# Optimization experiments

Measured on AMD Instinct MI355X. Metric: run time of the kernel, lower is better.

## Reference

```python
import jax, jax.numpy as jnp
import numpy as np

B, S, D, H = 2, 2048, 1024, 16
HD = D // H  # head_dim = 64


def setup_inputs() -> dict:
    key = jax.random.key(0)
    ks = jax.random.split(key, 10)
    std = 1.0 / np.sqrt(D)
    inputs = jax.random.normal(ks[0], (B, S, D), dtype=jnp.float32)
    # stacked per-head projection weights: [H, HD, D] (row-major like nn.Linear)
    Wq = jax.random.uniform(ks[1], (H, HD, D), jnp.float32, -std, std)
    bq = jax.random.uniform(ks[2], (H, HD), jnp.float32, -std, std)
    Wk = jax.random.uniform(ks[3], (H, HD, D), jnp.float32, -std, std)
    bk = jax.random.uniform(ks[4], (H, HD), jnp.float32, -std, std)
    Wv = jax.random.uniform(ks[5], (H, HD, D), jnp.float32, -std, std)
    bv = jax.random.uniform(ks[6], (H, HD), jnp.float32, -std, std)
    Wo = jax.random.uniform(ks[7], (D, D), jnp.float32, -std, std)
    bo = jax.random.uniform(ks[8], (D,), jnp.float32, -std, std)
    return {"inputs": inputs, "Wq": Wq, "bq": bq, "Wk": Wk, "bk": bk,
            "Wv": Wv, "bv": bv, "Wo": Wo, "bo": bo}


def reference(inputs, Wq, bq, Wk, bk, Wv, bv, Wo, bo):
    # per-head projections, batched over heads: [B,H,S,HD]
    q = jnp.einsum('bsd,hed->bhse', inputs, Wq) + bq[None, :, None, :]
    k = jnp.einsum('bsd,hed->bhse', inputs, Wk) + bk[None, :, None, :]
    v = jnp.einsum('bsd,hed->bhse', inputs, Wv) + bv[None, :, None, :]
    scale = 1.0 / np.sqrt(HD).astype(np.float32)
    # explicit [B,H,S,S] score matrix, as in the original naive attention
    scores = jnp.einsum('bhqe,bhke->bhqk', q, k) * scale
    causal = jnp.tril(jnp.ones((S, S), dtype=bool))
    scores = jnp.where(causal[None, None], scores, jnp.float32(-jnp.inf))
    attn = jax.nn.softmax(scores, axis=-1)  # dropout p=0 -> identity
    wv = jnp.einsum('bhqk,bhke->bhqe', attn, v)
    # concat heads along feature dim: [B,S,H*HD] = [B,S,D]
    z = wv.transpose(0, 2, 1, 3).reshape(B, S, D)
    out = jnp.einsum('bsd,ed->bse', z, Wo) + bo
    return out
```

## Files before the change

### kernel.cpp

```cpp
#include <hip/hip_runtime.h>
#include <math.h>

#define Bx 2
#define Sx 2048
#define Dx 1024
#define Hx 16
#define HDx 64
#define Mx (Bx*Sx)

typedef __bf16 bf16x8 __attribute__((ext_vector_type(8)));
typedef __bf16 bf16x4 __attribute__((ext_vector_type(4)));
typedef float  f32x4  __attribute__((ext_vector_type(4)));

#define SCL 0.18033688011112042f

__device__ __forceinline__ void gload_lds16(const __bf16* g, __bf16* l) {
  __builtin_amdgcn_global_load_lds(
      (const __attribute__((address_space(1))) unsigned int*)g,
      (__attribute__((address_space(3))) unsigned int*)l, 16, 0, 0);
}

__device__ __forceinline__ void cvt8(const float* s, __bf16* d) {
  float4 a = *(const float4*)s;
  float4 b = *(const float4*)(s + 4);
  bf16x8 o;
  o[0] = (__bf16)a.x; o[1] = (__bf16)a.y; o[2] = (__bf16)a.z; o[3] = (__bf16)a.w;
  o[4] = (__bf16)b.x; o[5] = (__bf16)b.y; o[6] = (__bf16)b.z; o[7] = (__bf16)b.w;
  *(bf16x8*)d = o;
}

__global__ __launch_bounds__(256) void cvt_kernel(
    const float* __restrict__ x, const float* __restrict__ Wq,
    const float* __restrict__ Wk, const float* __restrict__ Wv,
    const float* __restrict__ Wo, const float* __restrict__ bq,
    const float* __restrict__ bk, const float* __restrict__ bv,
    __bf16* __restrict__ xb, __bf16* __restrict__ wqkv,
    __bf16* __restrict__ wob, float* __restrict__ bqkv)
{
  const int bid = blockIdx.x;
  const int t = threadIdx.x;
  const size_t MEG = 1024u * 1024u;
  if (bid < 2048) {
    size_t e = (size_t)bid * 2048 + t * 8;
    cvt8(x + e, xb + e);
  } else if (bid < 3584) {
    size_t e = (size_t)(bid - 2048) * 2048 + t * 8;
    const float* src = (e < MEG) ? (Wq + e) : (e < 2 * MEG) ? (Wk + (e - MEG)) : (Wv + (e - 2 * MEG));
    cvt8(src, wqkv + e);
  } else if (bid < 4096) {
    size_t e = (size_t)(bid - 3584) * 2048 + t * 8;
    cvt8(Wo + e, wob + e);
  } else {
    for (int i = t; i < 3072; i += 256)
      bqkv[i] = (i < 1024) ? bq[i] : (i < 2048) ? bk[i - 1024] : bv[i - 2048];
  }
}

template<int TM, int TN, int MODE>
__global__ __launch_bounds__(256) void gemm_k(
    const __bf16* __restrict__ A, const __bf16* __restrict__ W,
    const float* __restrict__ bias, float* __restrict__ Cf,
    __bf16* __restrict__ Cb, __bf16* __restrict__ vT,
    int M, int N, int K, int ldc)
{
  __shared__ __align__(16) char smem[2 * (TM + TN) * 64 * 2];
  __bf16* AsB = (__bf16*)smem;

  constexpr int MS = TM / 32;
  constexpr int NS = TN / 32;
  const int tid = threadIdx.x;
  const int lane = tid & 63, wave = tid >> 6;
  const int l16 = lane & 15, quad = lane >> 4;
  const int wm = (wave >> 1) * (TM / 2);
  const int wn = (wave & 1) * (TN / 2);
  const int swz = l16 & 7;

  const int lid = blockIdx.y * gridDim.x + blockIdx.x;
  const int g8 = lid >> 6;
  const int r64 = lid & 63;
  const int gpm = (int)gridDim.y >> 3;
  const int gm = g8 % gpm;
  const int gn = g8 / gpm;
  const int m0 = (gm * 8 + (r64 & 7)) * TM;
  const int n0 = (gn * 8 + (r64 >> 3)) * TN;

  const f32x4 zero = {0.f, 0.f, 0.f, 0.f};
  f32x4 acc[MS][NS];
#pragma unroll
  for (int i = 0; i < MS; ++i)
#pragma unroll
    for (int j = 0; j < NS; ++j) acc[i][j] = zero;

  const int srow = tid >> 3;
  const int scs = (tid & 7) ^ (srow & 7);
  const __bf16* Ag = A + (size_t)(m0 + srow) * K + scs * 8;
  const __bf16* Wg = W + (size_t)(n0 + srow) * K + scs * 8;

#define G_STAGE(k0_, b_)                                                        \
  { __bf16* As_ = AsB + (b_) * (TM + TN) * 64;                                  \
    __bf16* Bs_ = As_ + TM * 64;                                                \
    _Pragma("unroll")                                                           \
    for (int i = 0; i < TM / 32; ++i)                                           \
      gload_lds16(Ag + (size_t)(i * 32) * K + (k0_), &As_[(i * 256 + tid) * 8]);\
    _Pragma("unroll")                                                           \
    for (int i = 0; i < TN / 32; ++i)                                           \
      gload_lds16(Wg + (size_t)(i * 32) * K + (k0_), &Bs_[(i * 256 + tid) * 8]); }

  const int NT = K >> 6;
  G_STAGE(0, 0)
  __syncthreads();

  for (int t = 0; t < NT; ++t) {
    if (t + 1 < NT) G_STAGE((t + 1) << 6, (t + 1) & 1)
    const __bf16* As_ = AsB + (t & 1) * (TM + TN) * 64;
    const __bf16* Bs_ = As_ + TM * 64;
#pragma unroll
    for (int hk = 0; hk < 2; ++hk) {
      const int ph = ((hk * 4 + quad) ^ swz) * 8;
      bf16x8 af[MS], bfr[NS];
#pragma unroll
      for (int i = 0; i < MS; ++i)
        af[i] = *(const bf16x8*)&As_[(wm + i * 16 + l16) * 64 + ph];
#pragma unroll
      for (int j = 0; j < NS; ++j)
        bfr[j] = *(const bf16x8*)&Bs_[(wn + j * 16 + l16) * 64 + ph];
#pragma unroll
      for (int i = 0; i < MS; ++i)
#pragma unroll
        for (int j = 0; j < NS; ++j)
          acc[i][j] = __builtin_amdgcn_mfma_f32_16x16x32_bf16(af[i], bfr[j], acc[i][j], 0, 0, 0);
    }
    __syncthreads();
  }

  if (MODE == 0) {
    float* Cs = (float*)smem;
    constexpr int cst = TN + 4;
#pragma unroll
    for (int j = 0; j < NS; ++j) {
      const int c = wn + j * 16 + l16;
      const float bv_ = bias[n0 + c];
#pragma unroll
      for (int i = 0; i < MS; ++i) {
        const int r0 = wm + i * 16 + quad * 4;
#pragma unroll
        for (int g = 0; g < 4; ++g)
          Cs[(r0 + g) * cst + c] = acc[i][j][g] + bv_;
      }
    }
    __syncthreads();
    constexpr int passes = TM * TN / (256 * 4);
#pragma unroll
    for (int p = 0; p < passes; ++p) {
      const int slot = p * 256 + tid;
      const int row = slot / (TN / 4);
      const int col4 = (slot % (TN / 4)) * 4;
      f32x4 v = *(const f32x4*)&Cs[row * cst + col4];
      *(f32x4*)&Cf[(size_t)(m0 + row) * ldc + n0 + col4] = v;
    }
  } else {
    __bf16* Cs = (__bf16*)smem;
    constexpr int cst = TN + 8;
    const bool vtile = (n0 >= 2048);
    if (!vtile) {
#pragma unroll
      for (int j = 0; j < NS; ++j) {
        const int c = wn + j * 16 + l16;
        const float bv_ = bias[n0 + c];
        const float sc = ((n0 + c) < 1024) ? SCL : 1.0f;
#pragma unroll
        for (int i = 0; i < MS; ++i) {
          const int r0 = wm + i * 16 + quad * 4;
#pragma unroll
          for (int g = 0; g < 4; ++g)
            Cs[(r0 + g) * cst + c] = (__bf16)((acc[i][j][g] + bv_) * sc);
        }
      }
      __syncthreads();
      constexpr int passes = TM * TN / (256 * 8);
#pragma unroll
      for (int p = 0; p < passes; ++p) {
        const int slot = p * 256 + tid;
        const int row = slot / (TN / 8);
        const int col8 = (slot % (TN / 8)) * 8;
        bf16x8 v = *(const bf16x8*)&Cs[row * cst + col8];
        *(bf16x8*)&Cb[(size_t)(m0 + row) * 3072 + n0 + col8] = v;
      }
    } else {
      constexpr int cstT = TM + 8;
#pragma unroll
      for (int j = 0; j < NS; ++j) {
        const int c = wn + j * 16 + l16;
        const float bv_ = bias[n0 + c];
#pragma unroll
        for (int i = 0; i < MS; ++i) {
          const int r0 = wm + i * 16 + quad * 4;
#pragma unroll
          for (int g = 0; g < 4; ++g)
            Cs[c * cstT + r0 + g] = (__bf16)(acc[i][j][g] + bv_);
        }
      }
      __syncthreads();
      const int bb = m0 >> 11, ml = m0 & 2047;
      constexpr int passes = TM * TN / (256 * 8);
#pragma unroll
      for (int p = 0; p < passes; ++p) {
        const int slot = p * 256 + tid;
        const int dd = slot / (TM / 8);
        const int ss8 = (slot % (TM / 8)) * 8;
        bf16x8 v = *(const bf16x8*)&Cs[dd * cstT + ss8];
        const int c2 = n0 - 2048 + dd;
        const int hh = c2 >> 6, ddd = c2 & 63;
        *(bf16x8*)&vT[((size_t)(bb * 16 + hh) * 64 + ddd) * 2048 + ml + ss8] = v;
      }
    }
  }
}

__global__ __launch_bounds__(256, 3) void attn_mfma(
    const __bf16* __restrict__ qkv, const __bf16* __restrict__ vT,
    __bf16* __restrict__ zb)
{
  __shared__ __bf16 Ks[3][64 * 64];
  __shared__ __bf16 Vs[3][64 * 64];

  const int tid = threadIdx.x;
  const int lane = tid & 63, wave = tid >> 6;
  const int l16 = lane & 15, quad = lane >> 4;
  const int bx = blockIdx.x;
  const int qt = 31 - (bx >> 5);
  const int bh = bx & 31;
  const int h = bh & 15, b = bh >> 4;
  const int q0 = qt * 64;

  const __bf16* qg = qkv + (size_t)b * 2048 * 3072 + h * 64;
  const __bf16* kg = qg + 1024;
  const __bf16* vg = vT + (size_t)bh * 64 * 2048;

#define STAGE_K(kt_, kbuf)                                                      \
  { const int kn = (kt_) * 64;                                                  \
    _Pragma("unroll")                                                           \
    for (int i = 0; i < 2; ++i) {                                               \
      int slot = i * 256 + tid;                                                 \
      int row = slot >> 3, ph2 = slot & 7;                                      \
      int cs = ph2 ^ (row & 7);                                                 \
      gload_lds16(kg + (size_t)(kn + row) * 3072 + cs * 8, &Ks[kbuf][slot * 8]);\
    } }

#define STAGE_V(kt_, vbuf)                                                      \
  { const int kn = (kt_) * 64;                                                  \
    _Pragma("unroll")                                                           \
    for (int i = 0; i < 2; ++i) {                                               \
      int slot = i * 256 + tid;                                                 \
      int row = slot >> 3, ph2 = slot & 7;                                      \
      int cs = ph2 ^ (row & 7);                                                 \
      gload_lds16(vg + (size_t)row * 2048 + kn + cs * 8, &Vs[vbuf][slot * 8]);  \
    } }

  const int swz = l16 & 7;
  const int sw0 = ((quad) ^ swz) * 8;
  const int sw1 = ((quad + 4) ^ swz) * 8;
  const int vcol = (((2 * wave + (quad >> 1)) ^ swz) * 8) + (quad & 1) * 4;
  const __bf16 ZB = (__bf16)0.0f;

  bf16x8 qf0[4], qf1[4];
#pragma unroll
  for (int n = 0; n < 4; ++n) {
    const __bf16* qr = qg + (size_t)(q0 + n * 16 + l16) * 3072;
    qf0[n] = *(const bf16x8*)&qr[quad * 8];
    qf1[n] = *(const bf16x8*)&qr[(quad + 4) * 8];
  }

  STAGE_V(0, 0)
  STAGE_K(0, 0)
  STAGE_K(1, 1)
  STAGE_V(1, 1)
  STAGE_K(2, 2)

  asm volatile("s_waitcnt vmcnt(4)" ::: "memory");
  __builtin_amdgcn_sched_barrier(0);
  __builtin_amdgcn_s_barrier();
  __builtin_amdgcn_sched_barrier(0);

  const f32x4 zero = {0.f, 0.f, 0.f, 0.f};
  f32x4 acc[4][4];
#pragma unroll
  for (int jt = 0; jt < 4; ++jt)
#pragma unroll
    for (int n = 0; n < 4; ++n) acc[jt][n] = zero;
  float lacc[4] = {0.f, 0.f, 0.f, 0.f};
  f32x4 s[4];
  bf16x8 pb[4];

#define S_TILE(kb)                                                              \
  { __builtin_amdgcn_s_setprio(1);                                              \
    bf16x8 kf0 = *(const bf16x8*)&Ks[kb][(wave * 16 + l16) * 64 + sw0];         \
    bf16x8 kf1 = *(const bf16x8*)&Ks[kb][(wave * 16 + l16) * 64 + sw1];         \
    _Pragma("unroll")                                                           \
    for (int n = 0; n < 4; ++n) {                                               \
      s[n] = zero;                                                              \
      s[n] = __builtin_amdgcn_mfma_f32_16x16x32_bf16(kf0, qf0[n], s[n], 0, 0, 0);\
      s[n] = __builtin_amdgcn_mfma_f32_16x16x32_bf16(kf1, qf1[n], s[n], 0, 0, 0);\
    }                                                                           \
    __builtin_amdgcn_s_setprio(0); }

  const int kqb = wave * 16 + quad * 4;

#define EXP_PB(DIAG)                                                            \
  { _Pragma("unroll")                                                           \
    for (int n = 0; n < 4; ++n) {                                               \
      const int ql = n * 16 + l16;                                              \
      float e0 = __builtin_exp2f(s[n][0]);                                      \
      float e1 = __builtin_exp2f(s[n][1]);                                      \
      float e2 = __builtin_exp2f(s[n][2]);                                      \
      float e3 = __builtin_exp2f(s[n][3]);                                      \
      if (DIAG) {                                                               \
        if (kqb + 0 > ql) e0 = 0.f;                                             \
        if (kqb + 1 > ql) e1 = 0.f;                                             \
        if (kqb + 2 > ql) e2 = 0.f;                                             \
        if (kqb + 3 > ql) e3 = 0.f;                                             \
      }                                                                         \
      pb[n] = (bf16x8){(__bf16)e0, (__bf16)e1, (__bf16)e2, (__bf16)e3,          \
                       ZB, ZB, ZB, ZB};                                         \
      lacc[n] += (e0 + e1) + (e2 + e3);                                         \
    } }

#define PV_TILE(vb)                                                             \
  { __builtin_amdgcn_s_setprio(1);                                              \
    _Pragma("unroll")                                                           \
    for (int jt = 0; jt < 4; ++jt) {                                            \
      bf16x4 vv = *(const bf16x4*)&Vs[vb][(jt * 16 + l16) * 64 + vcol];         \
      bf16x8 av = (bf16x8){vv[0], vv[1], vv[2], vv[3], ZB, ZB, ZB, ZB};         \
      _Pragma("unroll")                                                         \
      for (int n = 0; n < 4; ++n)                                               \
        acc[jt][n] = __builtin_amdgcn_mfma_f32_16x16x32_bf16(av, pb[n], acc[jt][n], 0, 0, 0); \
    }                                                                           \
    __builtin_amdgcn_s_setprio(0); }

  S_TILE(0)

  for (int t = 0; t < qt; ++t) {
    EXP_PB(false)
    const bool stV = (t + 2 <= qt);
    const bool stK = (t + 3 <= qt);
    if (stV) STAGE_V(t + 2, (t + 2) % 3)
    if (stK) STAGE_K(t + 3, (t + 3) % 3)
    S_TILE((t + 1) % 3)
    PV_TILE(t % 3)
    if (stV && stK)      asm volatile("s_waitcnt vmcnt(4)" ::: "memory");
    else if (stV || stK) asm volatile("s_waitcnt vmcnt(2)" ::: "memory");
    else                 asm volatile("s_waitcnt vmcnt(0)" ::: "memory");
    __builtin_amdgcn_sched_barrier(0);
    __builtin_amdgcn_s_barrier();
    __builtin_amdgcn_sched_barrier(0);
  }
  EXP_PB(true)
  PV_TILE(qt % 3)
  __syncthreads();

  float* redA = (float*)&Ks[0][0];
  float* redB = (float*)&Vs[0][0];
  float* lred = (float*)&Ks[2][0];
#pragma unroll
  for (int n = 0; n < 4; ++n) {
    float v = lacc[n];
    v += __shfl_xor(v, 16);
    v += __shfl_xor(v, 32);
    lacc[n] = v;
  }
  if (quad == 0) {
#pragma unroll
    for (int n = 0; n < 4; ++n) lred[wave * 64 + n * 16 + l16] = lacc[n];
  }

#define WR_ACC(dst)                                                             \
  { _Pragma("unroll")                                                           \
    for (int jt = 0; jt < 4; ++jt)                                              \
      _Pragma("unroll")                                                         \
      for (int n = 0; n < 4; ++n)                                               \
        *(f32x4*)&dst[(jt * 4 + n) * 256 + lane * 4] = acc[jt][n]; }
#define ADD_ACC(srcp)                                                           \
  { _Pragma("unroll")                                                           \
    for (int jt = 0; jt < 4; ++jt)                                              \
      _Pragma("unroll")                                                         \
      for (int n = 0; n < 4; ++n) {                                             \
        f32x4 tmp = *(const f32x4*)&srcp[(jt * 4 + n) * 256 + lane * 4];        \
        acc[jt][n] += tmp;                                                      \
      } }

  if (wave == 1) WR_ACC(redA)
  if (wave == 3) WR_ACC(redB)
  __syncthreads();
  if (wave == 0) ADD_ACC(redA)
  if (wave == 2) ADD_ACC(redB)
  __syncthreads();
  if (wave == 2) WR_ACC(redA)
  __syncthreads();
  if (wave == 0) {
    ADD_ACC(redA)
    float inv[4];
#pragma unroll
    for (int n = 0; n < 4; ++n) {
      const float lsum = lred[n * 16 + l16] + lred[64 + n * 16 + l16]
                       + lred[128 + n * 16 + l16] + lred[192 + n * 16 + l16];
      inv[n] = 1.0f / lsum;
    }
#pragma unroll
    for (int jt = 0; jt < 4; ++jt)
#pragma unroll
      for (int n = 0; n < 4; ++n) {
        bf16x4 ov = (bf16x4){(__bf16)(acc[jt][n][0] * inv[n]),
                             (__bf16)(acc[jt][n][1] * inv[n]),
                             (__bf16)(acc[jt][n][2] * inv[n]),
                             (__bf16)(acc[jt][n][3] * inv[n])};
        *(bf16x4*)&zb[(size_t)(b * 2048 + q0 + n * 16 + l16) * 1024
                      + h * 64 + jt * 16 + quad * 4] = ov;
      }
  }
}

extern "C" void kernel_launch(void* const* d_in, const int* in_sizes, int n_in,
                              void* d_out, int out_size, void* d_ws, size_t ws_size,
                              hipStream_t stream) {
  (void)in_sizes; (void)n_in; (void)out_size; (void)ws_size;
  const float* x  = (const float*)d_in[0];
  const float* Wq = (const float*)d_in[1];
  const float* bq = (const float*)d_in[2];
  const float* Wk = (const float*)d_in[3];
  const float* bk = (const float*)d_in[4];
  const float* Wv = (const float*)d_in[5];
  const float* bv = (const float*)d_in[6];
  const float* Wo = (const float*)d_in[7];
  const float* bo = (const float*)d_in[8];

  char* ws = (char*)d_ws;
  __bf16* xb   = (__bf16*)(ws);
  __bf16* wqkv = (__bf16*)(ws + (8ull  << 20));
  __bf16* wob  = (__bf16*)(ws + (14ull << 20));
  float*  bqkv = (float*) (ws + (16ull << 20));
  __bf16* qkv  = (__bf16*)(ws + (17ull << 20));
  __bf16* vT   = (__bf16*)(ws + (41ull << 20));
  __bf16* zb   = (__bf16*)(ws + (49ull << 20));

  cvt_kernel<<<4097, 256, 0, stream>>>(x, Wq, Wk, Wv, Wo, bq, bk, bv,
                                       xb, wqkv, wob, bqkv);
  gemm_k<128, 128, 1><<<dim3(24, 32), 256, 0, stream>>>(
      xb, wqkv, bqkv, nullptr, qkv, vT, Mx, 3072, 1024, 0);
  attn_mfma<<<1024, 256, 0, stream>>>(qkv, vT, zb);
  gemm_k<128, 64, 0><<<dim3(16, 32), 256, 0, stream>>>(
      zb, wob, bo, (float*)d_out, nullptr, nullptr, Mx, 1024, 1024, 1024);
}
```

Baseline: 184.9 us.

## Load K/V fragments directly from global memory into registers, dropping LDS staging

The attention kernel no longer stages K and V tiles through triple-buffered LDS with async global-to-LDS copies and per-iteration barriers. Each wave loads its own K rows and V columns straight into registers just before use, since no data was shared between waves. This removes the LDS round trip, the waitcnt bookkeeping and the block barriers, and shrinks shared memory to the reduction buffers. In exchange, global load latency is only hidden by a one-tile lookahead for K and none for V, so memory stalls may be more exposed.

After: 195.7 us. 5.8% more time.

```diff
diff --git a/kernel.cpp b/kernel.cpp
--- a/kernel.cpp
+++ b/kernel.cpp
@@ -169,7 +169,7 @@
         const float bv_ = bias[n0 + c];
         const float sc = ((n0 + c) < 1024) ? SCL : 1.0f;
 #pragma unroll
-        for (int i = 0; i < MS; ++i) {
+      for (int i = 0; i < MS; ++i) {
           const int r0 = wm + i * 16 + quad * 4;
 #pragma unroll
           for (int g = 0; g < 4; ++g)
@@ -221,8 +221,9 @@
     const __bf16* __restrict__ qkv, const __bf16* __restrict__ vT,
     __bf16* __restrict__ zb)
 {
-  __shared__ __bf16 Ks[3][64 * 64];
-  __shared__ __bf16 Vs[3][64 * 64];
+  __shared__ float redA[4096];
+  __shared__ float redB[4096];
+  __shared__ float lred[256];
 
   const int tid = threadIdx.x;
   const int lane = tid & 63, wave = tid >> 6;
@@ -237,30 +238,7 @@
   const __bf16* kg = qg + 1024;
   const __bf16* vg = vT + (size_t)bh * 64 * 2048;
 
-#define STAGE_K(kt_, kbuf)                                                      \
-  { const int kn = (kt_) * 64;                                                  \
-    _Pragma("unroll")                                                           \
-    for (int i = 0; i < 2; ++i) {                                               \
-      int slot = i * 256 + tid;                                                 \
-      int row = slot >> 3, ph2 = slot & 7;                                      \
-      int cs = ph2 ^ (row & 7);                                                 \
-      gload_lds16(kg + (size_t)(kn + row) * 3072 + cs * 8, &Ks[kbuf][slot * 8]);\
-    } }
-
-#define STAGE_V(kt_, vbuf)                                                      \
-  { const int kn = (kt_) * 64;                                                  \
-    _Pragma("unroll")                                                           \
-    for (int i = 0; i < 2; ++i) {                                               \
-      int slot = i * 256 + tid;                                                 \
-      int row = slot >> 3, ph2 = slot & 7;                                      \
-      int cs = ph2 ^ (row & 7);                                                 \
-      gload_lds16(vg + (size_t)row * 2048 + kn + cs * 8, &Vs[vbuf][slot * 8]);  \
-    } }
-
-  const int swz = l16 & 7;
-  const int sw0 = ((quad) ^ swz) * 8;
-  const int sw1 = ((quad + 4) ^ swz) * 8;
-  const int vcol = (((2 * wave + (quad >> 1)) ^ swz) * 8) + (quad & 1) * 4;
+  const __bf16* krow = kg + (size_t)(wave * 16 + l16) * 3072;
   const __bf16 ZB = (__bf16)0.0f;
 
   bf16x8 qf0[4], qf1[4];
@@ -271,17 +249,6 @@
     qf1[n] = *(const bf16x8*)&qr[(quad + 4) * 8];
   }
 
-  STAGE_V(0, 0)
-  STAGE_K(0, 0)
-  STAGE_K(1, 1)
-  STAGE_V(1, 1)
-  STAGE_K(2, 2)
-
-  asm volatile("s_waitcnt vmcnt(4)" ::: "memory");
-  __builtin_amdgcn_sched_barrier(0);
-  __builtin_amdgcn_s_barrier();
-  __builtin_amdgcn_sched_barrier(0);
-
   const f32x4 zero = {0.f, 0.f, 0.f, 0.f};
   f32x4 acc[4][4];
 #pragma unroll
@@ -291,11 +258,22 @@
   float lacc[4] = {0.f, 0.f, 0.f, 0.f};
   f32x4 s[4];
   bf16x8 pb[4];
-
-#define S_TILE(kb)                                                              \
+  bf16x4 vf[4];
+  bf16x8 kf0, kf1;
+
+#define LOAD_K(kt_)                                                             \
+  { const __bf16* kp = krow + (size_t)(kt_) * 64 * 3072;                        \
+    kf0 = *(const bf16x8*)&kp[quad * 8];                                        \
+    kf1 = *(const bf16x8*)&kp[(quad + 4) * 8]; }
+
+#define LOAD_V(kt_)                                                             \
+  { _Pragma("unroll")                                                           \
+    for (int jt = 0; jt < 4; ++jt)                                              \
+      vf[jt] = *(const bf16x4*)&vg[(size_t)(jt * 16 + l16) * 2048               \
+                                   + (kt_) * 64 + wave * 16 + quad * 4]; }
+
+#define S_TILE()                                                                \
   { __builtin_amdgcn_s_setprio(1);                                              \
-    bf16x8 kf0 = *(const bf16x8*)&Ks[kb][(wave * 16 + l16) * 64 + sw0];         \
-    bf16x8 kf1 = *(const bf16x8*)&Ks[kb][(wave * 16 + l16) * 64 + sw1];         \
     _Pragma("unroll")                                                           \
     for (int n = 0; n < 4; ++n) {                                               \
       s[n] = zero;                                                              \
@@ -325,42 +303,32 @@
       lacc[n] += (e0 + e1) + (e2 + e3);                                         \
     } }
 
-#define PV_TILE(vb)                                                             \
+#define PV_TILE()                                                               \
   { __builtin_amdgcn_s_setprio(1);                                              \
     _Pragma("unroll")                                                           \
     for (int jt = 0; jt < 4; ++jt) {                                            \
-      bf16x4 vv = *(const bf16x4*)&Vs[vb][(jt * 16 + l16) * 64 + vcol];         \
-      bf16x8 av = (bf16x8){vv[0], vv[1], vv[2], vv[3], ZB, ZB, ZB, ZB};         \
+      bf16x8 av = (bf16x8){vf[jt][0], vf[jt][1], vf[jt][2], vf[jt][3],          \
+                           ZB, ZB, ZB, ZB};                                     \
       _Pragma("unroll")                                                         \
       for (int n = 0; n < 4; ++n)                                               \
         acc[jt][n] = __builtin_amdgcn_mfma_f32_16x16x32_bf16(av, pb[n], acc[jt][n], 0, 0, 0); \
     }                                                                           \
     __builtin_amdgcn_s_setprio(0); }
 
-  S_TILE(0)
+  LOAD_K(0)
+  S_TILE()
 
   for (int t = 0; t < qt; ++t) {
+    LOAD_K(t + 1)
+    LOAD_V(t)
     EXP_PB(false)
-    const bool stV = (t + 2 <= qt);
-    const bool stK = (t + 3 <= qt);
-    if (stV) STAGE_V(t + 2, (t + 2) % 3)
-    if (stK) STAGE_K(t + 3, (t + 3) % 3)
-    S_TILE((t + 1) % 3)
-    PV_TILE(t % 3)
-    if (stV && stK)      asm volatile("s_waitcnt vmcnt(4)" ::: "memory");
-    else if (stV || stK) asm volatile("s_waitcnt vmcnt(2)" ::: "memory");
-    else                 asm volatile("s_waitcnt vmcnt(0)" ::: "memory");
-    __builtin_amdgcn_sched_barrier(0);
-    __builtin_amdgcn_s_barrier();
-    __builtin_amdgcn_sched_barrier(0);
-  }
+    S_TILE()
+    PV_TILE()
+  }
+  LOAD_V(qt)
   EXP_PB(true)
-  PV_TILE(qt % 3)
-  __syncthreads();
-
-  float* redA = (float*)&Ks[0][0];
-  float* redB = (float*)&Vs[0][0];
-  float* lred = (float*)&Ks[2][0];
+  PV_TILE()
+
 #pragma unroll
   for (int n = 0; n < 4; ++n) {
     float v = lacc[n];
```
